# Optimization experiments

Hardware: AMD Instinct MI355X
Metric: run time of the kernel (lower is better)

Reference implementation:

```python
import jax, jax.numpy as jnp
import numpy as np

N_EMBD = 1024
N_HEAD = 16
HEAD_DIM = N_EMBD // N_HEAD


def setup_inputs() -> dict:
    key = jax.random.key(0)
    ks = jax.random.split(key, 5)
    B, S = 2, 2048
    scale = 0.02
    return {
        "hidden_states": jax.random.normal(ks[0], (B, S, N_EMBD), dtype=jnp.float32),
        "w_attn": jax.random.normal(ks[1], (N_EMBD, 3 * N_EMBD), dtype=jnp.float32) * scale,
        "b_attn": jnp.zeros((3 * N_EMBD,), dtype=jnp.float32),
        "w_proj": jax.random.normal(ks[2], (N_EMBD, N_EMBD), dtype=jnp.float32) * scale,
        "b_proj": jnp.zeros((N_EMBD,), dtype=jnp.float32),
    }


def reference(hidden_states, w_attn, b_attn, w_proj, b_proj):
    B, S, _ = hidden_states.shape
    qkv = hidden_states @ w_attn + b_attn                     # [B,S,3E]
    q, k, v = jnp.split(qkv, 3, axis=-1)                      # each [B,S,E]

    def split_heads(t):  # [B,S,E] -> [B,H,S,D]
        return t.reshape(B, S, N_HEAD, HEAD_DIM).transpose(0, 2, 1, 3)

    q, k, v = split_heads(q), split_heads(k), split_heads(v)

    scores = jnp.einsum("bhqd,bhkd->bhqk", q, k) / np.sqrt(HEAD_DIM).astype(np.float32)
    causal = jnp.tril(jnp.ones((S, S), dtype=bool))
    scores = jnp.where(causal[None, None], scores, jnp.float32(-jnp.inf))
    attn = jax.nn.softmax(scores, axis=-1)                    # [B,H,S,S]
    out = jnp.einsum("bhqk,bhkd->bhqd", attn, v)              # [B,H,S,D]
    out = out.transpose(0, 2, 1, 3).reshape(B, S, N_EMBD)     # merge heads
    out = out @ w_proj + b_proj
    return out
```

## Files before the change

kernel.cpp:

```cpp
#include <hip/hip_runtime.h>
#include <hip/hip_bf16.h>


typedef __attribute__((ext_vector_type(4))) float  float4v;
typedef __attribute__((ext_vector_type(8))) short  short8v;
typedef __attribute__((ext_vector_type(4))) short  short4v;

#define ATT_SCALE 0.18033688011112042f

__device__ __forceinline__ short f2bf(float f) {
  union { float f; unsigned u; } v; v.f = f;
  unsigned r = v.u + 0x7fffu + ((v.u >> 16) & 1u);
  return (short)(r >> 16);
}
__device__ __forceinline__ float bf2f(short s) {
  union { unsigned u; float f; } v; v.u = ((unsigned)(unsigned short)s) << 16;
  return v.f;
}

__device__ __forceinline__ short4v pack_bf16x4(float a, float b, float c, float d) {
  unsigned x0 = __builtin_bit_cast(unsigned, a) + 0x8000u;
  unsigned x1 = __builtin_bit_cast(unsigned, b) + 0x8000u;
  unsigned x2 = __builtin_bit_cast(unsigned, c) + 0x8000u;
  unsigned x3 = __builtin_bit_cast(unsigned, d) + 0x8000u;
  union { unsigned u[2]; short4v s; } r;
  r.u[0] = __builtin_amdgcn_perm(x1, x0, 0x07060302);
  r.u[1] = __builtin_amdgcn_perm(x3, x2, 0x07060302);
  return r.s;
}

__device__ __forceinline__ void gl_lds16(const void* g, void* l) {
  __builtin_amdgcn_global_load_lds(
      (const __attribute__((address_space(1))) unsigned*)g,
      (__attribute__((address_space(3))) unsigned*)l, 16, 0, 0);
}

__global__ __launch_bounds__(256) void prep_kernel(
    const float* __restrict__ hidden, const float* __restrict__ w_attn,
    const float* __restrict__ w_proj, short* __restrict__ hA,
    short* __restrict__ wqkvT, short* __restrict__ wprojT) {
  __shared__ float tile[32][33];
  const int bx = blockIdx.x, t = threadIdx.x;
  if (bx < 4096) {
    const size_t i = ((size_t)bx * 256 + t) * 4;
    float4v v = *(const float4v*)(hidden + i);
    short4v o;
    #pragma unroll
    for (int k = 0; k < 4; k++) o[k] = f2bf(v[k]);
    *(short4v*)(hA + i) = o;
    return;
  }
  const float* in; short* out; int R, C, cx, cy;
  if (bx < 4096 + 3072) {
    in = w_attn; out = wqkvT; R = 1024; C = 3072;
    cx = (bx - 4096) % 96; cy = (bx - 4096) / 96;
  } else {
    in = w_proj; out = wprojT; R = 1024; C = 1024;
    cx = (bx - 7168) % 32; cy = (bx - 7168) / 32;
  }
  const int tx = t & 31, ty = t >> 5;
  const int c0 = cx * 32, r0 = cy * 32;
  #pragma unroll
  for (int i = 0; i < 4; i++)
    tile[ty + i * 8][tx] = in[(size_t)(r0 + ty + i * 8) * C + c0 + tx];
  __syncthreads();
  #pragma unroll
  for (int i = 0; i < 4; i++) {
    const int cc = ty + i * 8;
    out[(size_t)(c0 + cc) * R + r0 + tx] = f2bf(tile[tx][cc]);
  }
}

template<int RB, int MODE>
__global__ __launch_bounds__(256) void gemm_bt(
    const short* __restrict__ A, const short* __restrict__ Bt,
    const float* __restrict__ bias, void* __restrict__ Cout,
    short* __restrict__ vA, int M, int N, int K)
{
  __shared__ short As[2][RB][32];
  __shared__ short Bs[2][128][32];
  const int MI = RB / 32;
  const int t    = threadIdx.x;
  const int lane = t & 63;
  const int wave = t >> 6;
  const int wm   = (wave >> 1) * (RB / 2);
  const int wn   = (wave & 1) * 64;
  const int l16  = lane & 15;
  const int quad = lane >> 4;
  const int row0 = blockIdx.y * RB;
  const int col0 = blockIdx.x * 128;

  float4v acc[MI][4] = {};

  const int srow = lane >> 2;
  const int scol = (lane & 3) * 8;
  const int gcol = ((lane & 3) ^ ((srow >> 1) & 3)) * 8;
  const int rquad = (quad ^ ((l16 >> 1) & 3)) * 8;

  const short* gA0 = A + (size_t)(row0 + wave * ((RB == 128) ? 32 : 16) + srow) * K + gcol;
  const short* gA1 = gA0 + (size_t)16 * K;
  const short* gB0 = Bt + (size_t)(col0 + wave * 32 + srow) * K + gcol;
  const short* gB1 = gB0 + (size_t)16 * K;

  const int NI = K / 32;
  {
    if (RB == 128) {
      gl_lds16(gA0, &As[0][wave * 32 + srow][scol]);
      gl_lds16(gA1, &As[0][wave * 32 + 16 + srow][scol]);
    } else {
      gl_lds16(gA0, &As[0][(wave * 16 + srow) & (RB - 1)][scol]);
    }
    gl_lds16(gB0, &Bs[0][wave * 32 + srow][scol]);
    gl_lds16(gB1, &Bs[0][wave * 32 + 16 + srow][scol]);
  }

  for (int i = 0; i < NI; i++) {
    const int buf = i & 1;
    __syncthreads();
    if (i + 1 < NI) {
      const int k1 = (i + 1) * 32;
      if (RB == 128) {
        gl_lds16(gA0 + k1, &As[buf ^ 1][wave * 32 + srow][scol]);
        gl_lds16(gA1 + k1, &As[buf ^ 1][wave * 32 + 16 + srow][scol]);
      } else {
        gl_lds16(gA0 + k1, &As[buf ^ 1][(wave * 16 + srow) & (RB - 1)][scol]);
      }
      gl_lds16(gB0 + k1, &Bs[buf ^ 1][wave * 32 + srow][scol]);
      gl_lds16(gB1 + k1, &Bs[buf ^ 1][wave * 32 + 16 + srow][scol]);
    }
    short8v af[MI], bf[4];
    #pragma unroll
    for (int ii = 0; ii < MI; ii++)
      af[ii] = *(const short8v*)&As[buf][wm + ii * 16 + l16][rquad];
    #pragma unroll
    for (int j = 0; j < 4; j++)
      bf[j] = *(const short8v*)&Bs[buf][wn + j * 16 + l16][rquad];
    #pragma unroll
    for (int ii = 0; ii < MI; ii++)
      #pragma unroll
      for (int j = 0; j < 4; j++)
        acc[ii][j] = __builtin_amdgcn_mfma_f32_16x16x32_bf16(af[ii], bf[j], acc[ii][j], 0, 0, 0);
  }

  if (MODE == 2 && col0 >= 2048) {
    const int b  = row0 >> 11;
    const int hh = ((col0 - 2048) >> 6) + (wn >> 6);
    const int kt = ((row0 & 2047) >> 6) + (wm >> 6);
    short* vbase = vA + ((size_t)((b * 16 + hh) * 32 + kt) * 8) * 512;
    #pragma unroll
    for (int j = 0; j < 4; j++) {
      const float bv = bias[col0 + wn + j * 16 + l16];
      #pragma unroll
      for (int kwp = 0; kwp < 2; kwp++) {
        short8v s8;
        #pragma unroll
        for (int kw = 0; kw < 2; kw++) {
          short4v q4 = pack_bf16x4(acc[kwp * 2 + kw][j][0] + bv,
                                   acc[kwp * 2 + kw][j][1] + bv,
                                   acc[kwp * 2 + kw][j][2] + bv,
                                   acc[kwp * 2 + kw][j][3] + bv);
          #pragma unroll
          for (int r = 0; r < 4; r++) s8[kw * 4 + r] = q4[r];
        }
        *(short8v*)(vbase + ((size_t)(kwp * 4 + j) * 64 + lane) * 8) = s8;
      }
    }
    return;
  }

  #pragma unroll
  for (int j = 0; j < 4; j++) {
    const int col = col0 + wn + j * 16 + l16;
    const float sc = (MODE == 2 && col < 1024) ? ATT_SCALE : 1.0f;
    const float bv = bias[col];
    #pragma unroll
    for (int i = 0; i < MI; i++) {
      #pragma unroll
      for (int r = 0; r < 4; r++) {
        const int row = row0 + wm + i * 16 + quad * 4 + r;
        const float v = (acc[i][j][r] + bv) * sc;
        if (MODE == 2) ((short*)Cout)[(size_t)row * N + col] = f2bf(v);
        else           ((float*)Cout)[(size_t)row * N + col] = v;
      }
    }
  }
}

__global__ __launch_bounds__(256, 2) void attn_mfma(
    const short* __restrict__ qkv, const short* __restrict__ vA,
    short* __restrict__ P0, short* __restrict__ P1, float* __restrict__ lp)
{
  __shared__ short KA[2][8 * 512];
  __shared__ short VA[2][8 * 512];

  const int bh = blockIdx.y;
  const int b = bh >> 4, h = bh & 15;
  const int s = blockIdx.x;
  int qt = 0, sbase = 0;
  for (;;) { const int nc = (qt >> 3) + 1; if (s < sbase + nc) break; sbase += nc; qt++; }
  const int c = s - sbase;
  const int kt0  = c * 8;
  const int kend = min(qt + 1, kt0 + 8);

  const int t = threadIdx.x;
  const int lane = t & 63, w = t >> 6;
  const int l16 = lane & 15, quad = lane >> 4;

  const size_t base = (size_t)b * 2048 * 3072;
  const int qoff = h * 64, koff = 1024 + h * 64;
  const int qg = qt * 64 + w * 16 + l16;

  short8v qf[2];
  #pragma unroll
  for (int ks = 0; ks < 2; ks++)
    qf[ks] = *(const short8v*)(qkv + base + (size_t)qg * 3072 + qoff + ks * 32 + quad * 8);

  float4v O[4] = {};
  float l = 0.0f;

  const int id0 = w * 2, id1 = id0 + 1;
  const int jm0 = id0 & 3, ks0 = id0 >> 2;
  const int jm1 = id1 & 3, ks1 = id1 >> 2;
  const short* kg0 = qkv + base + (size_t)(jm0 * 16 + l16) * 3072 + koff + ks0 * 32 + quad * 8;
  const short* kg1 = qkv + base + (size_t)(jm1 * 16 + l16) * 3072 + koff + ks1 * 32 + quad * 8;
  const short* vg  = vA + (size_t)(bh * 32) * 4096 + lane * 8;

  gl_lds16(kg0 + (size_t)kt0 * 64 * 3072, &KA[0][id0 * 512 + lane * 8]);
  gl_lds16(kg1 + (size_t)kt0 * 64 * 3072, &KA[0][id1 * 512 + lane * 8]);
  gl_lds16(vg + (size_t)kt0 * 4096 + id0 * 512, &VA[0][id0 * 512 + lane * 8]);
  gl_lds16(vg + (size_t)kt0 * 4096 + id1 * 512, &VA[0][id1 * 512 + lane * 8]);

  for (int kt = kt0; kt < kend; kt++) {
    const int buf = (kt - kt0) & 1;
    __syncthreads();
    if (kt + 1 < kend) {
      gl_lds16(kg0 + (size_t)(kt + 1) * 64 * 3072, &KA[buf ^ 1][id0 * 512 + lane * 8]);
      gl_lds16(kg1 + (size_t)(kt + 1) * 64 * 3072, &KA[buf ^ 1][id1 * 512 + lane * 8]);
      gl_lds16(vg + (size_t)(kt + 1) * 4096 + id0 * 512, &VA[buf ^ 1][id0 * 512 + lane * 8]);
      gl_lds16(vg + (size_t)(kt + 1) * 4096 + id1 * 512, &VA[buf ^ 1][id1 * 512 + lane * 8]);
    }

    float4v sv[4] = {};
    #pragma unroll
    for (int ks = 0; ks < 2; ks++)
      #pragma unroll
      for (int jm = 0; jm < 4; jm++) {
        const short8v kf = *(const short8v*)&KA[buf][(ks * 4 + jm) * 512 + lane * 8];
        sv[jm] = __builtin_amdgcn_mfma_f32_16x16x32_bf16(kf, qf[ks], sv[jm], 0, 0, 0);
      }

    if (kt == qt) {
      #pragma unroll
      for (int jm = 0; jm < 4; jm++) {
        const int kv = kt * 64 + jm * 16 + quad * 4;
        #pragma unroll
        for (int r = 0; r < 4; r++)
          if (kv + r > qg) sv[jm][r] = -INFINITY;
      }
    }

    short4v pk[4];
    #pragma unroll
    for (int jm = 0; jm < 4; jm++) {
      float p0 = exp2f(sv[jm][0]), p1 = exp2f(sv[jm][1]);
      float p2 = exp2f(sv[jm][2]), p3 = exp2f(sv[jm][3]);
      l += (p0 + p1) + (p2 + p3);
      pk[jm] = pack_bf16x4(p0, p1, p2, p3);
    }

    #pragma unroll
    for (int id = 0; id < 8; id++) {
      const int kwp = id >> 2, dm = id & 3;
      const short8v vv = *(const short8v*)&VA[buf][id * 512 + lane * 8];
      const short4v v0 = {vv[0], vv[1], vv[2], vv[3]};
      const short4v v1 = {vv[4], vv[5], vv[6], vv[7]};
      O[dm] = __builtin_amdgcn_mfma_f32_16x16x16bf16_1k(v0, pk[kwp * 2],     O[dm], 0, 0, 0);
      O[dm] = __builtin_amdgcn_mfma_f32_16x16x16bf16_1k(v1, pk[kwp * 2 + 1], O[dm], 0, 0, 0);
    }
  }

  l += __shfl_xor(l, 16);
  l += __shfl_xor(l, 32);
  const int i = bh * 80 + s;
  short* pp = (i < 2048) ? (P0 + (size_t)i * 4096) : (P1 + (size_t)(i - 2048) * 4096);
  const int row = w * 16 + l16;
  if (quad == 0) lp[(size_t)i * 64 + row] = l;
  short* pr = pp + row * 64;
  #pragma unroll
  for (int dm = 0; dm < 4; dm++)
    *(short4v*)(pr + dm * 16 + quad * 4) =
        pack_bf16x4(O[dm][0], O[dm][1], O[dm][2], O[dm][3]);
}

__global__ __launch_bounds__(256) void merge_attn(
    const short* __restrict__ P0, const short* __restrict__ P1,
    const float* __restrict__ lp, short* __restrict__ aout)
{
  const int idx = blockIdx.x * 256 + threadIdx.x;
  const int q = idx >> 7;
  const int rest = idx & 127;
  const int h  = rest >> 3;
  const int dg = (rest & 7) * 8;
  const int b  = q >> 11;
  const int qr = q & 2047;
  const int qt = qr >> 6;
  const int row = qr & 63;
  const int a = qt >> 3, bq = qt & 7;
  const int off = qt + 4 * a * (a - 1) + a * bq;
  const int nc  = a + 1;
  const int bh  = b * 16 + h;

  float acc[8] = {};
  float suml = 0.0f;
  for (int c = 0; c < nc; c++) {
    const int i = bh * 80 + off + c;
    const short* pp = (i < 2048) ? (P0 + (size_t)i * 4096) : (P1 + (size_t)(i - 2048) * 4096);
    const short8v o = *(const short8v*)(pp + row * 64 + dg);
    #pragma unroll
    for (int k = 0; k < 8; k++) acc[k] += bf2f(o[k]);
    suml += lp[(size_t)i * 64 + row];
  }
  const float inv = 1.0f / suml;
  short8v ov;
  #pragma unroll
  for (int k = 0; k < 8; k++) ov[k] = f2bf(acc[k] * inv);
  *(short8v*)(aout + (size_t)q * 1024 + h * 64 + dg) = ov;
}

extern "C" void kernel_launch(void* const* d_in, const int* in_sizes, int n_in,
                              void* d_out, int out_size, void* d_ws, size_t ws_size,
                              hipStream_t stream) {
  const float* hidden = (const float*)d_in[0];
  const float* w_attn = (const float*)d_in[1];
  const float* b_attn = (const float*)d_in[2];
  const float* w_proj = (const float*)d_in[3];
  const float* b_proj = (const float*)d_in[4];
  float* outp = (float*)d_out;

  char* ws = (char*)d_ws;
  short* hA     = (short*)(ws);
  float* lp     = (float*)(ws + 8ull  * 1024 * 1024);
  short* wqkvT  = (short*)(ws + 8ull  * 1024 * 1024);
  short* wprojT = (short*)(ws + 14ull * 1024 * 1024);
  short* qkvb   = (short*)(ws + 16ull * 1024 * 1024);
  short* vAbuf  = (short*)(ws + 40ull * 1024 * 1024);
  short* aout   = (short*)(ws + 40ull * 1024 * 1024);
  short* P0     = (short*)d_out;

  prep_kernel<<<8192, 256, 0, stream>>>(hidden, w_attn, w_proj, hA, wqkvT, wprojT);
  gemm_bt<128, 2><<<dim3(24, 32), 256, 0, stream>>>(hA, wqkvT, b_attn, qkvb, vAbuf, 4096, 3072, 1024);
  attn_mfma<<<dim3(80, 32), 256, 0, stream>>>(qkvb, vAbuf, P0, hA, lp);
  merge_attn<<<2048, 256, 0, stream>>>(P0, hA, lp, aout);
  gemm_bt<64, 0><<<dim3(8, 64), 256, 0, stream>>>(aout, wprojT, b_proj, outp, nullptr, 4096, 1024, 1024);
}
```

Before: 205.5 us.

## Process two query tiles per attention block to reuse K/V loads

Each attention workgroup now handles 128 query rows (two 64-row groups) instead of 64, so every K/V tile staged in LDS feeds twice as many MFMAs. The split-K chunking, partial-output indexing and merge kernel are reworked to match, and the grid is halved. This halves the K/V global traffic and barrier count per unit of work. In exchange it raises register pressure (launch bounds changed to 3), adds branches for the diagonal handling, and gives fewer blocks for load balancing.

```diff
diff --git a/kernel.cpp b/kernel.cpp
--- a/kernel.cpp
+++ b/kernel.cpp
@@ -186,7 +186,7 @@
   }
 }
 
-__global__ __launch_bounds__(256, 2) void attn_mfma(
+__global__ __launch_bounds__(256, 3) void attn_mfma(
     const short* __restrict__ qkv, const short* __restrict__ vA,
     short* __restrict__ P0, short* __restrict__ P1, float* __restrict__ lp)
 {
@@ -197,10 +197,10 @@
   const int b = bh >> 4, h = bh & 15;
   const int s = blockIdx.x;
   int qt = 0, sbase = 0;
-  for (;;) { const int nc = (qt >> 3) + 1; if (s < sbase + nc) break; sbase += nc; qt++; }
+  for (;;) { const int nc = (2 * qt + 9) >> 3; if (s < sbase + nc) break; sbase += nc; qt++; }
   const int c = s - sbase;
   const int kt0  = c * 8;
-  const int kend = min(qt + 1, kt0 + 8);
+  const int kend = min(2 * qt + 2, kt0 + 8);
 
   const int t = threadIdx.x;
   const int lane = t & 63, w = t >> 6;
@@ -208,15 +208,19 @@
 
   const size_t base = (size_t)b * 2048 * 3072;
   const int qoff = h * 64, koff = 1024 + h * 64;
-  const int qg = qt * 64 + w * 16 + l16;
-
-  short8v qf[2];
-  #pragma unroll
-  for (int ks = 0; ks < 2; ks++)
-    qf[ks] = *(const short8v*)(qkv + base + (size_t)qg * 3072 + qoff + ks * 32 + quad * 8);
-
-  float4v O[4] = {};
-  float l = 0.0f;
+  int qg[2];
+  qg[0] = qt * 128 + w * 16 + l16;
+  qg[1] = qg[0] + 64;
+
+  short8v qf[2][2];
+  #pragma unroll
+  for (int g = 0; g < 2; g++)
+    #pragma unroll
+    for (int ks = 0; ks < 2; ks++)
+      qf[g][ks] = *(const short8v*)(qkv + base + (size_t)qg[g] * 3072 + qoff + ks * 32 + quad * 8);
+
+  float4v O[2][4] = {};
+  float l[2] = {0.0f, 0.0f};
 
   const int id0 = w * 2, id1 = id0 + 1;
   const int jm0 = id0 & 3, ks0 = id0 >> 2;
@@ -240,32 +244,53 @@
       gl_lds16(vg + (size_t)(kt + 1) * 4096 + id1 * 512, &VA[buf ^ 1][id1 * 512 + lane * 8]);
     }
 
-    float4v sv[4] = {};
+    const bool do0 = (kt <= 2 * qt);
+    float4v sv[2][4] = {};
     #pragma unroll
     for (int ks = 0; ks < 2; ks++)
       #pragma unroll
       for (int jm = 0; jm < 4; jm++) {
         const short8v kf = *(const short8v*)&KA[buf][(ks * 4 + jm) * 512 + lane * 8];
-        sv[jm] = __builtin_amdgcn_mfma_f32_16x16x32_bf16(kf, qf[ks], sv[jm], 0, 0, 0);
-      }
-
-    if (kt == qt) {
+        sv[1][jm] = __builtin_amdgcn_mfma_f32_16x16x32_bf16(kf, qf[1][ks], sv[1][jm], 0, 0, 0);
+        if (do0)
+          sv[0][jm] = __builtin_amdgcn_mfma_f32_16x16x32_bf16(kf, qf[0][ks], sv[0][jm], 0, 0, 0);
+      }
+
+    if (do0 && kt == 2 * qt) {
       #pragma unroll
       for (int jm = 0; jm < 4; jm++) {
         const int kv = kt * 64 + jm * 16 + quad * 4;
         #pragma unroll
         for (int r = 0; r < 4; r++)
-          if (kv + r > qg) sv[jm][r] = -INFINITY;
-      }
-    }
-
-    short4v pk[4];
+          if (kv + r > qg[0]) sv[0][jm][r] = -INFINITY;
+      }
+    }
+    if (kt == 2 * qt + 1) {
+      #pragma unroll
+      for (int jm = 0; jm < 4; jm++) {
+        const int kv = kt * 64 + jm * 16 + quad * 4;
+        #pragma unroll
+        for (int r = 0; r < 4; r++)
+          if (kv + r > qg[1]) sv[1][jm][r] = -INFINITY;
+      }
+    }
+
+    short4v pk[2][4];
     #pragma unroll
     for (int jm = 0; jm < 4; jm++) {
-      float p0 = exp2f(sv[jm][0]), p1 = exp2f(sv[jm][1]);
-      float p2 = exp2f(sv[jm][2]), p3 = exp2f(sv[jm][3]);
-      l += (p0 + p1) + (p2 + p3);
-      pk[jm] = pack_bf16x4(p0, p1, p2, p3);
+      float p0 = exp2f(sv[1][jm][0]), p1 = exp2f(sv[1][jm][1]);
+      float p2 = exp2f(sv[1][jm][2]), p3 = exp2f(sv[1][jm][3]);
+      l[1] += (p0 + p1) + (p2 + p3);
+      pk[1][jm] = pack_bf16x4(p0, p1, p2, p3);
+    }
+    if (do0) {
+      #pragma unroll
+      for (int jm = 0; jm < 4; jm++) {
+        float p0 = exp2f(sv[0][jm][0]), p1 = exp2f(sv[0][jm][1]);
+        float p2 = exp2f(sv[0][jm][2]), p3 = exp2f(sv[0][jm][3]);
+        l[0] += (p0 + p1) + (p2 + p3);
+        pk[0][jm] = pack_bf16x4(p0, p1, p2, p3);
+      }
     }
 
     #pragma unroll
@@ -274,22 +299,29 @@
       const short8v vv = *(const short8v*)&VA[buf][id * 512 + lane * 8];
       const short4v v0 = {vv[0], vv[1], vv[2], vv[3]};
       const short4v v1 = {vv[4], vv[5], vv[6], vv[7]};
-      O[dm] = __builtin_amdgcn_mfma_f32_16x16x16bf16_1k(v0, pk[kwp * 2],     O[dm], 0, 0, 0);
-      O[dm] = __builtin_amdgcn_mfma_f32_16x16x16bf16_1k(v1, pk[kwp * 2 + 1], O[dm], 0, 0, 0);
-    }
-  }
-
-  l += __shfl_xor(l, 16);
-  l += __shfl_xor(l, 32);
-  const int i = bh * 80 + s;
-  short* pp = (i < 2048) ? (P0 + (size_t)i * 4096) : (P1 + (size_t)(i - 2048) * 4096);
-  const int row = w * 16 + l16;
-  if (quad == 0) lp[(size_t)i * 64 + row] = l;
-  short* pr = pp + row * 64;
-  #pragma unroll
-  for (int dm = 0; dm < 4; dm++)
-    *(short4v*)(pr + dm * 16 + quad * 4) =
-        pack_bf16x4(O[dm][0], O[dm][1], O[dm][2], O[dm][3]);
+      O[1][dm] = __builtin_amdgcn_mfma_f32_16x16x16bf16_1k(v0, pk[1][kwp * 2],     O[1][dm], 0, 0, 0);
+      O[1][dm] = __builtin_amdgcn_mfma_f32_16x16x16bf16_1k(v1, pk[1][kwp * 2 + 1], O[1][dm], 0, 0, 0);
+      if (do0) {
+        O[0][dm] = __builtin_amdgcn_mfma_f32_16x16x16bf16_1k(v0, pk[0][kwp * 2],     O[0][dm], 0, 0, 0);
+        O[0][dm] = __builtin_amdgcn_mfma_f32_16x16x16bf16_1k(v1, pk[0][kwp * 2 + 1], O[0][dm], 0, 0, 0);
+      }
+    }
+  }
+
+  const int i = bh * 40 + s;
+  short* pp = (i < 1024) ? (P0 + (size_t)i * 8192) : (P1 + (size_t)(i - 1024) * 8192);
+  #pragma unroll
+  for (int g = 0; g < 2; g++) {
+    l[g] += __shfl_xor(l[g], 16);
+    l[g] += __shfl_xor(l[g], 32);
+    const int rowin = g * 64 + w * 16 + l16;
+    if (quad == 0) lp[(size_t)i * 128 + rowin] = l[g];
+    short* pr = pp + rowin * 64;
+    #pragma unroll
+    for (int dm = 0; dm < 4; dm++)
+      *(short4v*)(pr + dm * 16 + quad * 4) =
+          pack_bf16x4(O[g][dm][0], O[g][dm][1], O[g][dm][2], O[g][dm][3]);
+  }
 }
 
 __global__ __launch_bounds__(256) void merge_attn(
@@ -303,22 +335,22 @@
   const int dg = (rest & 7) * 8;
   const int b  = q >> 11;
   const int qr = q & 2047;
-  const int qt = qr >> 6;
-  const int row = qr & 63;
-  const int a = qt >> 3, bq = qt & 7;
-  const int off = qt + 4 * a * (a - 1) + a * bq;
-  const int nc  = a + 1;
+  const int qt = qr >> 7;
+  const int rowin = qr & 127;
+  const int g2 = qt >> 2, j2 = qt & 3;
+  const int off = (g2 + 1) * (2 * g2 + j2);
+  const int nc  = (2 * qt + 9) >> 3;
   const int bh  = b * 16 + h;
 
   float acc[8] = {};
   float suml = 0.0f;
   for (int c = 0; c < nc; c++) {
-    const int i = bh * 80 + off + c;
-    const short* pp = (i < 2048) ? (P0 + (size_t)i * 4096) : (P1 + (size_t)(i - 2048) * 4096);
-    const short8v o = *(const short8v*)(pp + row * 64 + dg);
+    const int i = bh * 40 + off + c;
+    const short* pp = (i < 1024) ? (P0 + (size_t)i * 8192) : (P1 + (size_t)(i - 1024) * 8192);
+    const short8v o = *(const short8v*)(pp + rowin * 64 + dg);
     #pragma unroll
     for (int k = 0; k < 8; k++) acc[k] += bf2f(o[k]);
-    suml += lp[(size_t)i * 64 + row];
+    suml += lp[(size_t)i * 128 + rowin];
   }
   const float inv = 1.0f / suml;
   short8v ov;
@@ -349,7 +381,7 @@
 
   prep_kernel<<<8192, 256, 0, stream>>>(hidden, w_attn, w_proj, hA, wqkvT, wprojT);
   gemm_bt<128, 2><<<dim3(24, 32), 256, 0, stream>>>(hA, wqkvT, b_attn, qkvb, vAbuf, 4096, 3072, 1024);
-  attn_mfma<<<dim3(80, 32), 256, 0, stream>>>(qkvb, vAbuf, P0, hA, lp);
+  attn_mfma<<<dim3(40, 32), 256, 0, stream>>>(qkvb, vAbuf, P0, hA, lp);
   merge_attn<<<2048, 256, 0, stream>>>(P0, hA, lp, aout);
   gemm_bt<64, 0><<<dim3(8, 64), 256, 0, stream>>>(aout, wprojT, b_proj, outp, nullptr, 4096, 1024, 1024);
 }
```

Measured after the change: 320.0 us. 1.56x slower.
